# Performance work log

Hardware: AMD Instinct MI355X
Metric: run time of the kernel (lower is better)

Reference implementation:

```python
import jax, jax.numpy as jnp
import numpy as np

H_FEAT, W_FEAT, K_ANCH = 512, 512, 9
FIELD = 32.0
IMG_W, IMG_H = int(W_FEAT * FIELD), int(H_FEAT * FIELD)
TOP_K = 4000          # pre-NMS candidate cap (fixed size for jit)
THRESHOLD = 0.5       # objectness threshold (call() default)
NMS_IOU = 0.3         # constructor default


def setup_inputs() -> dict:
    key = jax.random.key(0)
    k1, k2 = jax.random.split(key)
    output_obj = jax.random.normal(k1, (H_FEAT, W_FEAT, 2 * K_ANCH), jnp.float32)
    output_reg = jax.random.normal(k2, (H_FEAT, W_FEAT, 4 * K_ANCH), jnp.float32) * 0.05
    anchor_px = jnp.array([16, 32, 48, 64, 96, 128, 192, 256, 384], jnp.int32)
    # create_anchors: square anchors centered on each feature-map cell
    ys, xs = jnp.meshgrid(jnp.arange(H_FEAT, dtype=jnp.float32),
                          jnp.arange(W_FEAT, dtype=jnp.float32), indexing='ij')
    cx = (xs + 0.5) * FIELD            # [H, W]
    cy = (ys + 0.5) * FIELD
    w = anchor_px.astype(jnp.float32)  # [K]
    ax = cx[:, :, None] - w[None, None, :] / 2.0   # [H, W, K]
    ay = cy[:, :, None] - w[None, None, :] / 2.0
    aw = jnp.broadcast_to(w[None, None, :], (H_FEAT, W_FEAT, K_ANCH))
    anchors = jnp.stack([ax, ay, aw, aw], axis=-1).reshape(-1, 4)  # [H*W*K, 4]
    return {"output_obj": output_obj, "output_reg": output_reg,
            "anchors": anchors, "anchor_px": anchor_px}


def map_outputs(output, anchors, anchor_px):
    # vectorized version of per-anchor tf.map_fn(argmax) + gather_nd
    K = anchor_px.shape[0]
    idx = jnp.argmax(anchors[:, 3:4].astype(jnp.int32) == anchor_px[None, :], axis=1)
    px = ((anchors[:, 0] + anchors[:, 2] / 2.0) / FIELD).astype(jnp.int32)
    py = ((anchors[:, 1] + anchors[:, 3] / 2.0) / FIELD).astype(jnp.int32)
    D = output.shape[-1] // K
    reshaped = output.reshape(output.shape[0], output.shape[1], K, D)
    return reshaped[py, px, idx]   # [H*W*K, D]


def unparameterize(reg, anchors):
    cx = anchors[:, 0] + anchors[:, 2] / 2.0 + reg[:, 0] * anchors[:, 2]
    cy = anchors[:, 1] + anchors[:, 3] / 2.0 + reg[:, 1] * anchors[:, 3]
    w = anchors[:, 2] * jnp.exp(reg[:, 2])
    h = anchors[:, 3] * jnp.exp(reg[:, 3])
    return jnp.stack([cx - w / 2.0, cy - h / 2.0, w, h], axis=1)


def clip_boxes(boxes, width, height):
    x1 = jnp.clip(boxes[:, 0], 0.0, width)
    y1 = jnp.clip(boxes[:, 1], 0.0, height)
    x2 = jnp.clip(boxes[:, 0] + boxes[:, 2], 0.0, width)
    y2 = jnp.clip(boxes[:, 1] + boxes[:, 3], 0.0, height)
    return jnp.stack([x1, y1, x2 - x1, y2 - y1], axis=1)


def forward(output_obj, output_reg, anchors, anchor_px):
    rpn_obj = jax.nn.softmax(map_outputs(output_obj, anchors, anchor_px), axis=-1)
    rpn_reg = map_outputs(output_reg, anchors, anchor_px)
    rpn_boxes = clip_boxes(unparameterize(rpn_reg, anchors), float(IMG_W), float(IMG_H))
    scores = rpn_obj[:, 1]
    # threshold(): boolean_mask -> realized as score masking + fixed-size top-k
    masked = jnp.where(scores > THRESHOLD, scores, -1.0)
    top_scores, top_idx = jax.lax.top_k(masked, TOP_K)
    b = rpn_boxes[top_idx]        # [TOP_K, 4], sorted by score desc
    o = rpn_obj[top_idx]          # [TOP_K, 2]
    valid = top_scores > THRESHOLD
    # pairwise IoU in corner form
    x1, y1 = b[:, 0], b[:, 1]
    x2, y2 = x1 + b[:, 2], y1 + b[:, 3]
    area = b[:, 2] * b[:, 3]
    iw = jnp.clip(jnp.minimum(x2[:, None], x2[None, :]) - jnp.maximum(x1[:, None], x1[None, :]), 0.0)
    ih = jnp.clip(jnp.minimum(y2[:, None], y2[None, :]) - jnp.maximum(y1[:, None], y1[None, :]), 0.0)
    inter = iw * ih
    iou = inter / (area[:, None] + area[None, :] - inter + 1e-8)
    rng = jnp.arange(TOP_K)
    # greedy NMS over score-sorted candidates (tf.image.non_max_suppression)
    def body(i, keep):
        sup = (iou[i] > NMS_IOU) & (rng > i) & keep[i]
        return keep & jnp.logical_not(sup)
    keep = jax.lax.fori_loop(0, TOP_K, body, valid)
    return b, o, keep


def reference(output_obj, output_reg, anchors, anchor_px):
    return forward(output_obj, output_reg, anchors, anchor_px)
```

## Files before the change

kernel.cpp:

```cpp
#include <hip/hip_runtime.h>
#include <cstdint>
#include <math.h>

#pragma clang fp contract(off)

typedef unsigned int u32;
typedef unsigned long long u64;

#define HFEAT 512
#define WFEAT 512
#define NPIX (HFEAT*WFEAT)
#define NANCH (NPIX*9)
#define TOPK 4000
#define IMG_SZ 16384.0f
#define NBUCKET 8192
#define CAP 32768
#define NWORD 63
#define RCACHE 224
#define COARSE_CUT (-3.5f)
#define COARSE_BUK_SAFE 1537

#define WS_META 32768
#define WS_SUP  32832
#define WS_VALM 33344
#define WS_CKEY 33856
#define WS_SEL  296000
#define WS_NX1  312000
#define WS_NY1  328000
#define WS_NX2  344000
#define WS_NY2  360000
#define WS_NAR  376000
#define WS_VAL  392000
#define WS_MASK 408000
#define WS_RANK WS_MASK
#define WS_COARSE (WS_MASK + 131072)
#define WS_DIAG 2456000

__device__ __forceinline__ int dbucket_bits(u32 bits) {
    int b = (int)((bits - 0xC0000000u) >> 12);
    return (b > (NBUCKET - 1)) ? (NBUCKET - 1) : b;
}

__device__ __forceinline__ float score1(float d) {
    float e0 = (float)::exp((double)d);
    float den = e0 + 1.0f;
    return 1.0f / den;
}

__device__ __forceinline__ void softmax2(float l0, float l1, float& s0, float& s1) {
    float m = fmaxf(l0, l1);
    float a0 = l0 - m;
    float a1 = l1 - m;
    float e0 = (float)::exp((double)a0);
    float e1 = (float)::exp((double)a1);
    float den = e0 + e1;
    s0 = e0 / den;
    s1 = e1 / den;
}

__global__ void k_zero(u32* ws32) {
    int t = blockIdx.x * blockDim.x + threadIdx.x;
    if (t < 272) ws32[WS_META/4 + t] = 0;
    if (t < CAP) ws32[WS_RANK/4 + t] = 0;
}

__global__ void k_coarse(const float* __restrict__ obj, u64* __restrict__ coarse,
                         u32* __restrict__ meta) {
    __shared__ u64 stage[512];
    __shared__ u32 scnt, sbase;
    int tid = threadIdx.x;
    if (tid == 0) scnt = 0;
    __syncthreads();
    const float2* o2 = (const float2*)obj;
    int base = blockIdx.x * (256 * 9);
#pragma unroll
    for (int k = 0; k < 9; ++k) {
        int a = base + k * 256 + tid;
        float2 v = o2[a];
        float d = v.x - v.y;
        if (d < COARSE_CUT) {
            u32 p = atomicAdd(&scnt, 1u);
            if (p < 512) stage[p] = ((u64)__float_as_uint(d) << 32) | (u32)a;
        }
    }
    __syncthreads();
    u32 cntr = scnt;
    u32 cnt = (cntr > 512u) ? 512u : cntr;
    if (tid == 0 && cntr) {
        sbase = atomicAdd(&meta[3], (cntr > 512u) ? (u32)CAP : cnt);
    }
    __syncthreads();
    if (cnt)
        for (u32 t = tid; t < cnt; t += 256) {
            u32 pos = sbase + t;
            if (pos < CAP) coarse[pos] = stage[t];
        }
}

__global__ __launch_bounds__(1024) void k_select(const u64* __restrict__ coarse,
                                                 u32* __restrict__ meta) {
    __shared__ u32 lh[NBUCKET];
    __shared__ u32 ss[1024];
    int tid = threadIdx.x;
    for (int b = tid; b < NBUCKET; b += 1024) lh[b] = 0;
    __syncthreads();
    u32 coarseN = meta[3];
    bool ok = (coarseN >= (u32)TOPK) && (coarseN < (u32)CAP);
    if (ok) {
        for (u32 t = tid; t < coarseN; t += 1024) {
            u32 dbits = (u32)(coarse[t] >> 32);
            atomicAdd(&lh[dbucket_bits(dbits)], 1u);
        }
    }
    __syncthreads();
    u32 local = 0;
#pragma unroll
    for (int j = 0; j < 8; ++j) local += lh[tid*8 + j];
    ss[tid] = local;
    __syncthreads();
    for (int off = 1; off < 1024; off <<= 1) {
        u32 v = (tid + off < 1024) ? ss[tid + off] : 0;
        __syncthreads();
        ss[tid] += v;
        __syncthreads();
    }
    if (!ok) { if (tid == 0) { meta[1] = 0; meta[5] = 0; } return; }
    u32 S_t = ss[tid];
    u32 S_next = (tid < 1023) ? ss[tid+1] : 0;
    if (S_t >= TOPK && S_next < TOPK) {
        u32 cum = S_next;
        int bsel = tid*8;
        for (int b = tid*8 + 7; b >= tid*8; --b) {
            cum += lh[b];
            if (cum >= TOPK) { bsel = b; break; }
        }
        u32 thr = (u32)((bsel > 0) ? bsel - 1 : 0);
        meta[1] = thr;
        meta[2] = cum;
        meta[5] = (thr >= COARSE_BUK_SAFE) ? 1u : 0u;
    }
}

__global__ void k_key(const float* __restrict__ obj, u32* __restrict__ meta,
                      const u64* __restrict__ coarse, u64* __restrict__ ckeyp) {
    __shared__ u64 stage[256];
    __shared__ u32 scnt, sbase;
    int tid = threadIdx.x;
    if (tid == 0) scnt = 0;
    __syncthreads();
    bool fast = meta[5] != 0u;
    if (fast) {
        u32 coarseN = meta[3];
        int thr = (int)meta[1];
        u32 t = blockIdx.x * 256 + tid;
        if (blockIdx.x * 256 < coarseN) {
            if (t < coarseN) {
                u64 e = coarse[t];
                u32 dbits = (u32)(e >> 32);
                if (dbucket_bits(dbits) >= thr) {
                    float s1 = score1(__uint_as_float(dbits));
                    u32 bits = __float_as_uint(s1);
                    u32 p = atomicAdd(&scnt, 1u);
                    stage[p] = ((u64)bits << 32) | (u32)(~(u32)(e & 0xFFFFFFFFull));
                }
            }
            __syncthreads();
            u32 cnt = scnt;
            if (tid == 0 && cnt) sbase = atomicAdd(&meta[0], cnt);
            __syncthreads();
            if (cnt && tid < cnt) {
                u32 pos = sbase + tid;
                if (pos < CAP) ckeyp[pos] = stage[tid];
            }
        }
    } else {
        const float2* o2 = (const float2*)obj;
        for (int a = blockIdx.x * 256 + tid; a < NANCH; a += gridDim.x * 256) {
            float2 v = o2[a];
            float d = v.x - v.y;
            if (d < 0.0f) {
                float s1 = score1(d);
                if (s1 > 0.5f) {
                    u32 bits = __float_as_uint(s1);
                    u32 pos = atomicAdd(&meta[0], 1u);
                    if (pos < CAP) ckeyp[pos] = ((u64)bits << 32) | (u32)(~(u32)a);
                }
            }
        }
    }
}

#define RSL 1024
#define NSLICE 4
__global__ void k_rank(const u32* __restrict__ meta, const u64* __restrict__ ckeyp,
                       u32* __restrict__ rankbuf) {
    __shared__ u64 lk[RSL];
    int tid = threadIdx.x;
    u32 Mu = meta[0];
    int M = (int)(Mu < (u32)CAP ? Mu : (u32)CAP);
    int c = blockIdx.y * 256 + tid;
    if (blockIdx.y * 256 >= M) return;
    bool act = (c < M);
    u64 mypk = act ? ckeyp[c] : 0ull;
    int cnt = 0;
    for (int t0 = blockIdx.x * RSL; t0 < M; t0 += NSLICE * RSL) {
        __syncthreads();
        for (int j = tid; j < RSL; j += 256)
            lk[j] = (t0 + j < M) ? ckeyp[t0 + j] : 0ull;
        __syncthreads();
#pragma unroll 16
        for (int j = 0; j < RSL; ++j)
            cnt += (lk[j] > mypk) ? 1 : 0;
    }
    if (act && cnt) atomicAdd(&rankbuf[c], (u32)cnt);
}

__global__ void k_sel(const u32* __restrict__ meta, const u64* __restrict__ ckeyp,
                      const u32* __restrict__ rankbuf, u32* __restrict__ sel) {
    u32 Mu = meta[0];
    int M = (int)(Mu < (u32)CAP ? Mu : (u32)CAP);
    int c = blockIdx.x * 256 + threadIdx.x;
    if (c >= M) return;
    u32 r = rankbuf[c];
    if (r < TOPK) sel[r] = ~(u32)(ckeyp[c] & 0xFFFFFFFFull);
}

__global__ void k_gather(const float* __restrict__ obj, const float* __restrict__ reg,
                         const float* __restrict__ anch, const u32* __restrict__ sel,
                         float* __restrict__ out,
                         float* __restrict__ nx1, float* __restrict__ ny1,
                         float* __restrict__ nx2, float* __restrict__ ny2,
                         float* __restrict__ nar, u32* __restrict__ valid,
                         u64* __restrict__ valm) {
    int r = blockIdx.x * 256 + threadIdx.x;
    if (r >= TOPK) return;
    u32 i = sel[r];
    u32 p = i / 9u, k = i - p * 9u;
    float l0 = obj[(size_t)p*18 + 2*k];
    float l1 = obj[(size_t)p*18 + 2*k + 1];
    float s0, s1;
    softmax2(l0, l1, s0, s1);
    const float* rg = reg + (size_t)p*36 + 4*k;
    float t0 = rg[0], t1 = rg[1], t2 = rg[2], t3 = rg[3];
    const float* an = anch + (size_t)i*4;
    float a0 = an[0], a1 = an[1], a2 = an[2], a3 = an[3];
    float cx = a0 + a2/2.0f + t0*a2;
    float cy = a1 + a3/2.0f + t1*a3;
    float w = a2 * (float)::exp((double)t2);
    float h = a3 * (float)::exp((double)t3);
    float bx = cx - w/2.0f;
    float by = cy - h/2.0f;
    float x1 = fminf(fmaxf(bx, 0.0f), IMG_SZ);
    float y1 = fminf(fmaxf(by, 0.0f), IMG_SZ);
    float x2 = fminf(fmaxf(bx + w, 0.0f), IMG_SZ);
    float y2 = fminf(fmaxf(by + h, 0.0f), IMG_SZ);
    float bw = x2 - x1, bh = y2 - y1;
    out[4*r+0] = x1;
    out[4*r+1] = y1;
    out[4*r+2] = bw;
    out[4*r+3] = bh;
    out[16000 + 2*r]     = s0;
    out[16000 + 2*r + 1] = s1;
    nx1[r] = x1; ny1[r] = y1;
    nx2[r] = x1 + bw;
    ny2[r] = y1 + bh;
    nar[r] = bw * bh;
    u32 vld = (s1 > 0.5f) ? 1u : 0u;
    valid[r] = vld;
    u64 bm = __ballot(vld != 0u);
    if ((threadIdx.x & 63) == 0) valm[r >> 6] = bm;
}

__device__ __forceinline__ bool iou_gt(float x1a, float y1a, float x2a, float y2a, float aA,
                                       float x1b, float y1b, float x2b, float y2b, float aB) {
    float iw = fminf(x2a, x2b) - fmaxf(x1a, x1b);
    float ih = fminf(y2a, y2b) - fmaxf(y1a, y1b);
    iw = fmaxf(iw, 0.0f);
    ih = fmaxf(ih, 0.0f);
    float inter = iw * ih;
    float iou = inter / (aA + aB - inter + 1e-8f);
    return iou > 0.3f;
}

__global__ void k_mask(const float* __restrict__ nx1, const float* __restrict__ ny1,
                       const float* __restrict__ nx2, const float* __restrict__ ny2,
                       const float* __restrict__ nar, u64* __restrict__ mask,
                       u64* __restrict__ diag, u64* __restrict__ supany) {
    __shared__ float cx1[64], cy1[64], cx2[64], cy2[64], car[64];
    int w = blockIdx.y;
    int j0 = w * 64;
    int tid = threadIdx.x;
    int i = blockIdx.x * 256 + tid;
    if (j0 + 63 < (int)(blockIdx.x * 256)) {
        if (i < TOPK) mask[(size_t)i * 64 + w] = 0ull;
        return;
    }
    if (tid < 64) {
        int j = j0 + tid;
        bool v = j < TOPK;
        cx1[tid] = v ? nx1[j] : 1e9f;
        cy1[tid] = v ? ny1[j] : 1e9f;
        cx2[tid] = v ? nx2[j] : 1e9f;
        cy2[tid] = v ? ny2[j] : 1e9f;
        car[tid] = v ? nar[j] : 0.f;
    }
    __syncthreads();
    if (i >= TOPK) return;
    float x1 = nx1[i], y1 = ny1[i], x2 = nx2[i], y2 = ny2[i], ar = nar[i];
    u64 bits = 0;
#pragma unroll
    for (int b = 0; b < 64; ++b) {
        int j = j0 + b;
        if (j < TOPK && j > i &&
            iou_gt(x1, y1, x2, y2, ar, cx1[b], cy1[b], cx2[b], cy2[b], car[b]))
            bits |= (1ull << b);
    }
    mask[(size_t)i * 64 + w] = bits;
    if (w == (i >> 6)) diag[i] = bits;
    u64 anyb = __ballot(bits != 0ull);
    if ((tid & 63) == 0 && anyb) atomicOr(&supany[i >> 6], anyb);
}

__global__ __launch_bounds__(512) void k_scan_nms(const u64* __restrict__ mask,
                                                  const u64* __restrict__ diag,
                                                  const u64* __restrict__ supany,
                                                  const u64* __restrict__ valm,
                                                  float* __restrict__ out) {
    __shared__ u64 dlds[NWORD * 64];
    __shared__ u64 cache[RCACHE * 64];
    __shared__ u32 rowlist[RCACHE];
    __shared__ u32 nrows_s;
    __shared__ u64 keep_s[64];
    int tid = threadIdx.x;
    int wave = tid >> 6, lane = tid & 63;

    for (int t = tid; t < NWORD * 64; t += 512)
        dlds[t] = (t < TOPK) ? diag[t] : 0ull;

    int excl = 0;
    u64 sa = 0;
    if (wave == 0) {
        sa = supany[lane];
        int c = (int)__popcll(sa);
        int pfx = c;
        for (int off = 1; off < 64; off <<= 1) {
            int n = __shfl_up(pfx, off);
            if (lane >= off) pfx += n;
        }
        excl = pfx - c;
        int total = __shfl(pfx, 63);
        if (lane == 0) nrows_s = (u32)((total < RCACHE) ? total : RCACHE);
        int s = excl; u64 t = sa;
        while (t) {
            int b = (int)__builtin_ctzll(t); t &= t - 1;
            if (s < RCACHE) rowlist[s] = (u32)((lane << 6) | b);
            s++;
        }
    }
    __syncthreads();
    int R = (int)nrows_s;
    {
        const int TW = RCACHE * 64;
        for (int t0 = tid; t0 < TW; t0 += 512 * 8) {
            u64 v[8];
#pragma unroll
            for (int u = 0; u < 8; ++u) {
                int t = t0 + u * 512;
                int sl = t >> 6;
                int row = (t < TW && sl < R) ? (int)rowlist[sl] : 0;
                v[u] = (t < TW) ? mask[(size_t)row * 64 + (t & 63)] : 0ull;
            }
#pragma unroll
            for (int u = 0; u < 8; ++u) {
                int t = t0 + u * 512;
                if (t < TW) cache[t] = v[u];
            }
        }
    }
    __syncthreads();
    if (wave == 0) {
        u64 kw = valm[lane];
        u64 gm = __ballot((sa & kw) != 0ull);
        while (gm) {
            int g = (int)__builtin_ctzll(gm); gm &= gm - 1;
            u64 wg  = __shfl(kw, g);
            u64 sag = __shfl(sa, g);
            u64 supAlive = wg & sag;
            if (supAlive == 0ull) continue;
            int sbase = __shfl(excl, g);
            u64 dg = dlds[(g << 6) | lane];
            u64 am = wg, act = supAlive, keptSup = 0ull;
            while (act) {
                int s = (int)__builtin_ctzll(act);
                u64 sup = __shfl(dg, s);
                am &= ~sup;
                keptSup |= (1ull << s);
                act &= ~(1ull << s);
                act &= am;
            }
            u64 acc = 0, t = keptSup;
            while (t) {
                int s1b = (int)__builtin_ctzll(t); t &= t - 1;
                int sl1 = sbase + (int)__popcll(sag & ((1ull << s1b) - 1ull));
                if (t) {
                    int s2b = (int)__builtin_ctzll(t); t &= t - 1;
                    int sl2 = sbase + (int)__popcll(sag & ((1ull << s2b) - 1ull));
                    u64 ra = (sl1 < RCACHE) ? cache[(sl1 << 6) | lane]
                                            : mask[(size_t)((g << 6) | s1b) * 64 + lane];
                    u64 rb = (sl2 < RCACHE) ? cache[(sl2 << 6) | lane]
                                            : mask[(size_t)((g << 6) | s2b) * 64 + lane];
                    acc |= ra | rb;
                } else {
                    acc |= (sl1 < RCACHE) ? cache[(sl1 << 6) | lane]
                                          : mask[(size_t)((g << 6) | s1b) * 64 + lane];
                }
            }
            kw &= ~acc;
        }
        keep_s[lane] = kw;
    }
    __syncthreads();
    for (int t = tid; t < TOPK; t += 512)
        out[24000 + t] = ((keep_s[t >> 6] >> (t & 63)) & 1ull) ? 1.0f : 0.0f;
}

extern "C" void kernel_launch(void* const* d_in, const int* in_sizes, int n_in,
                              void* d_out, int out_size, void* d_ws, size_t ws_size,
                              hipStream_t stream) {
    const float* obj  = (const float*)d_in[0];
    const float* reg  = (const float*)d_in[1];
    const float* anch = (const float*)d_in[2];
    float* out = (float*)d_out;
    char* ws = (char*)d_ws;

    u32* meta = (u32*)(ws + WS_META);
    u64* supany = (u64*)(ws + WS_SUP);
    u64* valm = (u64*)(ws + WS_VALM);
    u64* ckeyp = (u64*)(ws + WS_CKEY);
    u32* sel  = (u32*)(ws + WS_SEL);
    float* nx1 = (float*)(ws + WS_NX1);
    float* ny1 = (float*)(ws + WS_NY1);
    float* nx2 = (float*)(ws + WS_NX2);
    float* ny2 = (float*)(ws + WS_NY2);
    float* nar = (float*)(ws + WS_NAR);
    u32* valid = (u32*)(ws + WS_VAL);
    u64* mask  = (u64*)(ws + WS_MASK);
    u64* diag  = (u64*)(ws + WS_DIAG);
    u32* rankbuf = (u32*)(ws + WS_RANK);
    u64* coarse  = (u64*)(ws + WS_COARSE);

    hipLaunchKernelGGL(k_zero, dim3((CAP + 255) / 256), dim3(256), 0, stream, (u32*)ws);
    hipLaunchKernelGGL(k_coarse, dim3(NANCH / (256*9)), dim3(256), 0, stream, obj, coarse, meta);
    hipLaunchKernelGGL(k_select, dim3(1), dim3(1024), 0, stream, coarse, meta);
    hipLaunchKernelGGL(k_key, dim3(CAP/256), dim3(256), 0, stream, obj, meta, coarse, ckeyp);
    hipLaunchKernelGGL(k_rank, dim3(NSLICE, CAP/256), dim3(256), 0, stream, meta, ckeyp, rankbuf);
    hipLaunchKernelGGL(k_sel, dim3(CAP/256), dim3(256), 0, stream, meta, ckeyp, rankbuf, sel);
    hipLaunchKernelGGL(k_gather, dim3((TOPK + 255) / 256), dim3(256), 0, stream,
                       obj, reg, anch, sel, out, nx1, ny1, nx2, ny2, nar, valid, valm);
    hipLaunchKernelGGL(k_mask, dim3((TOPK + 255) / 256, 64), dim3(256), 0, stream,
                       nx1, ny1, nx2, ny2, nar, mask, diag, supany);
    hipLaunchKernelGGL(k_scan_nms, dim3(1), dim3(512), 0, stream, mask, diag, supany, valm, out);
}
```

Baseline: 101.3 us.

## Fuse select/key and sel/gather kernels, vectorize coarse scan, drop rank zeroing

```diff
diff --git a/kernel.cpp b/kernel.cpp
--- a/kernel.cpp
+++ b/kernel.cpp
@@ -22,9 +22,7 @@
 
 #define WS_META 32768
 #define WS_SUP  32832
-#define WS_VALM 33344
 #define WS_CKEY 33856
-#define WS_SEL  296000
 #define WS_NX1  312000
 #define WS_NY1  328000
 #define WS_NX2  344000
@@ -33,7 +31,7 @@
 #define WS_VAL  392000
 #define WS_MASK 408000
 #define WS_RANK WS_MASK
-#define WS_COARSE (WS_MASK + 131072)
+#define WS_COARSE (WS_MASK + 524288)
 #define WS_DIAG 2456000
 
 __device__ __forceinline__ int dbucket_bits(u32 bits) {
@@ -59,28 +57,31 @@
 }
 
 __global__ void k_zero(u32* ws32) {
-    int t = blockIdx.x * blockDim.x + threadIdx.x;
-    if (t < 272) ws32[WS_META/4 + t] = 0;
-    if (t < CAP) ws32[WS_RANK/4 + t] = 0;
-}
-
-__global__ void k_coarse(const float* __restrict__ obj, u64* __restrict__ coarse,
+    int t = threadIdx.x;
+    if (t < 144) ws32[WS_META/4 + t] = 0;
+}
+
+__global__ void k_coarse(const float4* __restrict__ o4, u64* __restrict__ coarse,
                          u32* __restrict__ meta) {
     __shared__ u64 stage[512];
     __shared__ u32 scnt, sbase;
     int tid = threadIdx.x;
     if (tid == 0) scnt = 0;
     __syncthreads();
-    const float2* o2 = (const float2*)obj;
-    int base = blockIdx.x * (256 * 9);
+    int base = blockIdx.x * 2304;
 #pragma unroll
     for (int k = 0; k < 9; ++k) {
-        int a = base + k * 256 + tid;
-        float2 v = o2[a];
-        float d = v.x - v.y;
-        if (d < COARSE_CUT) {
+        int a4 = base + k * 256 + tid;
+        float4 v = o4[a4];
+        float d0 = v.x - v.y;
+        float d1 = v.z - v.w;
+        if (d0 < COARSE_CUT) {
             u32 p = atomicAdd(&scnt, 1u);
-            if (p < 512) stage[p] = ((u64)__float_as_uint(d) << 32) | (u32)a;
+            if (p < 512) stage[p] = ((u64)__float_as_uint(d0) << 32) | (u32)(2*a4);
+        }
+        if (d1 < COARSE_CUT) {
+            u32 p = atomicAdd(&scnt, 1u);
+            if (p < 512) stage[p] = ((u64)__float_as_uint(d1) << 32) | (u32)(2*a4 + 1);
         }
     }
     __syncthreads();
@@ -97,20 +98,23 @@
         }
 }
 
-__global__ __launch_bounds__(1024) void k_select(const u64* __restrict__ coarse,
-                                                 u32* __restrict__ meta) {
+__global__ __launch_bounds__(1024) void k_selectkey(const float* __restrict__ obj,
+                                                    u32* __restrict__ meta,
+                                                    const u64* __restrict__ coarse,
+                                                    u64* __restrict__ ckeyp) {
     __shared__ u32 lh[NBUCKET];
     __shared__ u32 ss[1024];
+    __shared__ u32 ps[1024];
+    __shared__ u32 thr_s;
     int tid = threadIdx.x;
     for (int b = tid; b < NBUCKET; b += 1024) lh[b] = 0;
+    if (tid == 0) thr_s = 0;
     __syncthreads();
     u32 coarseN = meta[3];
     bool ok = (coarseN >= (u32)TOPK) && (coarseN < (u32)CAP);
     if (ok) {
-        for (u32 t = tid; t < coarseN; t += 1024) {
-            u32 dbits = (u32)(coarse[t] >> 32);
-            atomicAdd(&lh[dbucket_bits(dbits)], 1u);
-        }
+        for (u32 t = tid; t < coarseN; t += 1024)
+            atomicAdd(&lh[dbucket_bits((u32)(coarse[t] >> 32))], 1u);
     }
     __syncthreads();
     u32 local = 0;
@@ -124,69 +128,60 @@
         ss[tid] += v;
         __syncthreads();
     }
-    if (!ok) { if (tid == 0) { meta[1] = 0; meta[5] = 0; } return; }
-    u32 S_t = ss[tid];
-    u32 S_next = (tid < 1023) ? ss[tid+1] : 0;
-    if (S_t >= TOPK && S_next < TOPK) {
-        u32 cum = S_next;
-        int bsel = tid*8;
-        for (int b = tid*8 + 7; b >= tid*8; --b) {
-            cum += lh[b];
-            if (cum >= TOPK) { bsel = b; break; }
-        }
-        u32 thr = (u32)((bsel > 0) ? bsel - 1 : 0);
-        meta[1] = thr;
-        meta[2] = cum;
-        meta[5] = (thr >= COARSE_BUK_SAFE) ? 1u : 0u;
-    }
-}
-
-__global__ void k_key(const float* __restrict__ obj, u32* __restrict__ meta,
-                      const u64* __restrict__ coarse, u64* __restrict__ ckeyp) {
-    __shared__ u64 stage[256];
-    __shared__ u32 scnt, sbase;
-    int tid = threadIdx.x;
-    if (tid == 0) scnt = 0;
-    __syncthreads();
-    bool fast = meta[5] != 0u;
+    if (ok) {
+        u32 S_t = ss[tid];
+        u32 S_next = (tid < 1023) ? ss[tid+1] : 0;
+        if (S_t >= TOPK && S_next < TOPK) {
+            u32 cum = S_next;
+            int bsel = tid*8;
+            for (int b = tid*8 + 7; b >= tid*8; --b) {
+                cum += lh[b];
+                if (cum >= TOPK) { bsel = b; break; }
+            }
+            thr_s = (u32)((bsel > 0) ? bsel - 1 : 0);
+        }
+    }
+    __syncthreads();
+    bool fast = ok && (thr_s >= (u32)COARSE_BUK_SAFE);
     if (fast) {
-        u32 coarseN = meta[3];
-        int thr = (int)meta[1];
-        u32 t = blockIdx.x * 256 + tid;
-        if (blockIdx.x * 256 < coarseN) {
-            if (t < coarseN) {
-                u64 e = coarse[t];
-                u32 dbits = (u32)(e >> 32);
-                if (dbucket_bits(dbits) >= thr) {
-                    float s1 = score1(__uint_as_float(dbits));
-                    u32 bits = __float_as_uint(s1);
-                    u32 p = atomicAdd(&scnt, 1u);
-                    stage[p] = ((u64)bits << 32) | (u32)(~(u32)(e & 0xFFFFFFFFull));
-                }
-            }
+        int thr = (int)thr_s;
+        u32 mycnt = 0;
+        for (u32 t = tid; t < coarseN; t += 1024)
+            if (dbucket_bits((u32)(coarse[t] >> 32)) >= thr) mycnt++;
+        ps[tid] = mycnt;
+        __syncthreads();
+        for (int off = 1; off < 1024; off <<= 1) {
+            u32 v = (tid >= off) ? ps[tid - off] : 0;
             __syncthreads();
-            u32 cnt = scnt;
-            if (tid == 0 && cnt) sbase = atomicAdd(&meta[0], cnt);
+            ps[tid] += v;
             __syncthreads();
-            if (cnt && tid < cnt) {
-                u32 pos = sbase + tid;
-                if (pos < CAP) ckeyp[pos] = stage[tid];
-            }
-        }
+        }
+        u32 w = ps[tid] - mycnt;
+        for (u32 t = tid; t < coarseN; t += 1024) {
+            u64 e = coarse[t];
+            u32 dbits = (u32)(e >> 32);
+            if (dbucket_bits(dbits) >= thr) {
+                float s1 = score1(__uint_as_float(dbits));
+                ckeyp[w++] = ((u64)__float_as_uint(s1) << 32) |
+                             (u32)(~(u32)(e & 0xFFFFFFFFull));
+            }
+        }
+        if (tid == 0) { meta[0] = ps[1023]; meta[1] = thr_s; meta[5] = 1u; }
     } else {
         const float2* o2 = (const float2*)obj;
-        for (int a = blockIdx.x * 256 + tid; a < NANCH; a += gridDim.x * 256) {
+        for (int a = tid; a < NANCH; a += 1024) {
             float2 v = o2[a];
             float d = v.x - v.y;
             if (d < 0.0f) {
                 float s1 = score1(d);
                 if (s1 > 0.5f) {
-                    u32 bits = __float_as_uint(s1);
                     u32 pos = atomicAdd(&meta[0], 1u);
-                    if (pos < CAP) ckeyp[pos] = ((u64)bits << 32) | (u32)(~(u32)a);
+                    if (pos < CAP)
+                        ckeyp[pos] = ((u64)__float_as_uint(s1) << 32) | (u32)(~(u32)a);
                 }
             }
         }
+        if (tid == 0) meta[5] = 0u;
     }
 }
 
@@ -212,29 +207,23 @@
         for (int j = 0; j < RSL; ++j)
             cnt += (lk[j] > mypk) ? 1 : 0;
     }
-    if (act && cnt) atomicAdd(&rankbuf[c], (u32)cnt);
-}
-
-__global__ void k_sel(const u32* __restrict__ meta, const u64* __restrict__ ckeyp,
-                      const u32* __restrict__ rankbuf, u32* __restrict__ sel) {
+    rankbuf[blockIdx.x * CAP + c] = (u32)cnt;
+}
+
+__global__ void k_selgather(const u32* __restrict__ meta, const u64* __restrict__ ckeyp,
+                            const u32* __restrict__ rankbuf,
+                            const float* __restrict__ obj, const float* __restrict__ reg,
+                            const float* __restrict__ anch, float* __restrict__ out,
+                            float* __restrict__ nx1, float* __restrict__ ny1,
+                            float* __restrict__ nx2, float* __restrict__ ny2,
+                            float* __restrict__ nar, u32* __restrict__ valid) {
     u32 Mu = meta[0];
     int M = (int)(Mu < (u32)CAP ? Mu : (u32)CAP);
     int c = blockIdx.x * 256 + threadIdx.x;
     if (c >= M) return;
-    u32 r = rankbuf[c];
-    if (r < TOPK) sel[r] = ~(u32)(ckeyp[c] & 0xFFFFFFFFull);
-}
-
-__global__ void k_gather(const float* __restrict__ obj, const float* __restrict__ reg,
-                         const float* __restrict__ anch, const u32* __restrict__ sel,
-                         float* __restrict__ out,
-                         float* __restrict__ nx1, float* __restrict__ ny1,
-                         float* __restrict__ nx2, float* __restrict__ ny2,
-                         float* __restrict__ nar, u32* __restrict__ valid,
-                         u64* __restrict__ valm) {
-    int r = blockIdx.x * 256 + threadIdx.x;
+    u32 r = rankbuf[c] + rankbuf[CAP + c] + rankbuf[2*CAP + c] + rankbuf[3*CAP + c];
     if (r >= TOPK) return;
-    u32 i = sel[r];
+    u32 i = ~(u32)(ckeyp[c] & 0xFFFFFFFFull);
     u32 p = i / 9u, k = i - p * 9u;
     float l0 = obj[(size_t)p*18 + 2*k];
     float l1 = obj[(size_t)p*18 + 2*k + 1];
@@ -265,10 +254,7 @@
     nx2[r] = x1 + bw;
     ny2[r] = y1 + bh;
     nar[r] = bw * bh;
-    u32 vld = (s1 > 0.5f) ? 1u : 0u;
-    valid[r] = vld;
-    u64 bm = __ballot(vld != 0u);
-    if ((threadIdx.x & 63) == 0) valm[r >> 6] = bm;
+    valid[r] = (s1 > 0.5f) ? 1u : 0u;
 }
 
 __device__ __forceinline__ bool iou_gt(float x1a, float y1a, float x2a, float y2a, float aA,
@@ -324,16 +310,23 @@
 __global__ __launch_bounds__(512) void k_scan_nms(const u64* __restrict__ mask,
                                                   const u64* __restrict__ diag,
                                                   const u64* __restrict__ supany,
-                                                  const u64* __restrict__ valm,
+                                                  const u32* __restrict__ valid,
                                                   float* __restrict__ out) {
     __shared__ u64 dlds[NWORD * 64];
     __shared__ u64 cache[RCACHE * 64];
     __shared__ u32 rowlist[RCACHE];
     __shared__ u32 nrows_s;
+    __shared__ u64 vml[64];
     __shared__ u64 keep_s[64];
     int tid = threadIdx.x;
     int wave = tid >> 6, lane = tid & 63;
 
+    for (int g = wave; g < 64; g += 8) {
+        int t = g * 64 + lane;
+        u32 v = (t < TOPK) ? valid[t] : 0u;
+        u64 bm = __ballot(v != 0u);
+        if (lane == 0) vml[g] = bm;
+    }
     for (int t = tid; t < NWORD * 64; t += 512)
         dlds[t] = (t < TOPK) ? diag[t] : 0ull;
 
@@ -379,7 +372,7 @@
     }
     __syncthreads();
     if (wave == 0) {
-        u64 kw = valm[lane];
+        u64 kw = vml[lane];
         u64 gm = __ballot((sa & kw) != 0ull);
         while (gm) {
             int g = (int)__builtin_ctzll(gm); gm &= gm - 1;
@@ -435,9 +428,7 @@
 
     u32* meta = (u32*)(ws + WS_META);
     u64* supany = (u64*)(ws + WS_SUP);
-    u64* valm = (u64*)(ws + WS_VALM);
     u64* ckeyp = (u64*)(ws + WS_CKEY);
-    u32* sel  = (u32*)(ws + WS_SEL);
     float* nx1 = (float*)(ws + WS_NX1);
     float* ny1 = (float*)(ws + WS_NY1);
     float* nx2 = (float*)(ws + WS_NX2);
@@ -449,15 +440,15 @@
     u32* rankbuf = (u32*)(ws + WS_RANK);
     u64* coarse  = (u64*)(ws + WS_COARSE);
 
-    hipLaunchKernelGGL(k_zero, dim3((CAP + 255) / 256), dim3(256), 0, stream, (u32*)ws);
-    hipLaunchKernelGGL(k_coarse, dim3(NANCH / (256*9)), dim3(256), 0, stream, obj, coarse, meta);
-    hipLaunchKernelGGL(k_select, dim3(1), dim3(1024), 0, stream, coarse, meta);
-    hipLaunchKernelGGL(k_key, dim3(CAP/256), dim3(256), 0, stream, obj, meta, coarse, ckeyp);
+    hipLaunchKernelGGL(k_zero, dim3(1), dim3(256), 0, stream, (u32*)ws);
+    hipLaunchKernelGGL(k_coarse, dim3(NANCH / 4608), dim3(256), 0, stream,
+                       (const float4*)obj, coarse, meta);
+    hipLaunchKernelGGL(k_selectkey, dim3(1), dim3(1024), 0, stream, obj, meta, coarse, ckeyp);
     hipLaunchKernelGGL(k_rank, dim3(NSLICE, CAP/256), dim3(256), 0, stream, meta, ckeyp, rankbuf);
-    hipLaunchKernelGGL(k_sel, dim3(CAP/256), dim3(256), 0, stream, meta, ckeyp, rankbuf, sel);
-    hipLaunchKernelGGL(k_gather, dim3((TOPK + 255) / 256), dim3(256), 0, stream,
-                       obj, reg, anch, sel, out, nx1, ny1, nx2, ny2, nar, valid, valm);
+    hipLaunchKernelGGL(k_selgather, dim3(CAP/256), dim3(256), 0, stream,
+                       meta, ckeyp, rankbuf, obj, reg, anch, out,
+                       nx1, ny1, nx2, ny2, nar, valid);
     hipLaunchKernelGGL(k_mask, dim3((TOPK + 255) / 256, 64), dim3(256), 0, stream,
                        nx1, ny1, nx2, ny2, nar, mask, diag, supany);
-    hipLaunchKernelGGL(k_scan_nms, dim3(1), dim3(512), 0, stream, mask, diag, supany, valm, out);
-}
+    hipLaunchKernelGGL(k_scan_nms, dim3(1), dim3(512), 0, stream, mask, diag, supany, valid, out);
+}
```

New measurement: 106.1 us. 4.8% more time.
